# Kernel optimization log

Hardware: AMD Instinct MI355X
Metric: run time of the kernel (lower is better)

The kernel has to match this reference:

```python
import jax, jax.numpy as jnp
import numpy as np

B, T, H, W = 32, 100, 16, 16
CIN, HID, COUT, K = 64, 128, 64, 5
EPS = 1e-3      # keras LayerNormalization default epsilon
ALPHA = 0.2     # LeakyReLU slope


def _conv_same(x, w):
    # x: [B,H,W,Cin], w: [kh,kw,Cin,Cout] -> [B,H,W,Cout], SAME padding, stride 1
    return jax.lax.conv_general_dilated(
        x, w, window_strides=(1, 1), padding='SAME',
        dimension_numbers=('NHWC', 'HWIO', 'NHWC'))


def setup_inputs() -> dict:
    key = jax.random.key(0)
    ks = jax.random.split(key, 8)
    s = 0.05
    return {
        'initial_input': jax.random.normal(ks[0], (B, 1, H, W, CIN), jnp.float32),
        'h0': jax.random.normal(ks[1], (B, H, W, HID), jnp.float32) * s,
        'c0': jax.random.normal(ks[2], (B, H, W, HID), jnp.float32) * s,
        'targets': jax.random.normal(ks[3], (B, T, H, W, CIN), jnp.float32),
        'autoreg_prob': jnp.float32(0.5),
        # ConvLSTM2D params (keras gate order: i, f, c, o stacked on last axis)
        'Wx': jax.random.normal(ks[4], (K, K, CIN, 4 * HID), jnp.float32) * s,
        'Wh': jax.random.normal(ks[5], (K, K, HID, 4 * HID), jnp.float32) * s,
        'b': jnp.zeros((4 * HID,), jnp.float32),
        # Conv2D(64, 3, same)
        'conv_w': jax.random.normal(ks[6], (3, 3, HID, COUT), jnp.float32) * s,
        'conv_b': jnp.zeros((COUT,), jnp.float32),
        # LayerNorm (axis=-1)
        'gamma': jnp.ones((COUT,), jnp.float32),
        'beta': jnp.zeros((COUT,), jnp.float32),
    }


def reference(initial_input, h0, c0, targets, autoreg_prob,
              Wx, Wh, b, conv_w, conv_b, gamma, beta):
    T_ = targets.shape[1]
    t_switch = jnp.float32(T_) * autoreg_prob
    x0 = initial_input[:, 0]                       # [B,H,W,CIN] (seq-len-1 ConvLSTM step)
    tgt_t = jnp.transpose(targets, (1, 0, 2, 3, 4))  # [T,B,H,W,CIN]
    ts = jnp.arange(T_)

    def step(carry, inp):
        x, h, c = carry
        t, tgt = inp
        # ConvLSTM2D cell (one timestep)
        g = _conv_same(x, Wx) + _conv_same(h, Wh) + b   # [B,H,W,4*HID]
        i_g, f_g, c_g, o_g = jnp.split(g, 4, axis=-1)
        c = jax.nn.sigmoid(f_g) * c + jax.nn.sigmoid(i_g) * jnp.tanh(c_g)
        h = jax.nn.sigmoid(o_g) * jnp.tanh(c)
        # Conv2D -> LayerNorm(axis=-1) -> LeakyReLU(0.2)
        y = _conv_same(h, conv_w) + conv_b              # [B,H,W,COUT]
        mu = jnp.mean(y, axis=-1, keepdims=True)
        var = jnp.var(y, axis=-1, keepdims=True)
        y = (y - mu) * jax.lax.rsqrt(var + EPS) * gamma + beta
        out = jnp.where(y >= 0, y, ALPHA * y)
        # autoreg phase feeds output back; teacher phase feeds targets[:, t]
        next_x = jnp.where(t.astype(jnp.float32) < t_switch, out, tgt)
        return (next_x, h, c), out

    _, outs = jax.lax.scan(step, (x0, h0, c0), (ts, tgt_t))
    return jnp.transpose(outs, (1, 0, 2, 3, 4))        # [B,T,H,W,COUT]
```

## Files before the change

### kernel.cpp

```cpp
#include <hip/hip_runtime.h>

#define TT   100
#define PADW 20
#define HID  128
#define CIN  64
#define COUT 64
#define ALPHA 0.2f
#define LNEPS 1e-3f

typedef _Float16 f16;
typedef __attribute__((ext_vector_type(8))) _Float16 f16x8;
typedef __attribute__((ext_vector_type(4))) float f32x4;

__device__ __forceinline__ float fsig(float x) {
  return __builtin_amdgcn_rcpf(1.f + __builtin_amdgcn_exp2f(-1.44269504089f * x));
}
__device__ __forceinline__ float ftanh(float x) {
  return 1.f - 2.f * __builtin_amdgcn_rcpf(1.f + __builtin_amdgcn_exp2f(2.88539008178f * x));
}
__device__ __forceinline__ void gload16(const void* g, void* l) {
  __builtin_amdgcn_global_load_lds((const __attribute__((address_space(1))) void*)g,
                                   (__attribute__((address_space(3))) void*)l,
                                   16, 0, 0);
}

__global__ __launch_bounds__(512, 1) void kA8(
    const f16* __restrict__ Xh, const f16* __restrict__ Xl,
    const f16* __restrict__ Hch, const f16* __restrict__ Hcl,
    f16* __restrict__ Hnh, f16* __restrict__ Hnl,
    const f16* __restrict__ Wch, const f16* __restrict__ Wcl,
    const float* __restrict__ bp, float* __restrict__ cst) {
  __shared__ __align__(16) char smem[126976];
  f16* haloh = (f16*)(smem);
  f16* halol = (f16*)(smem + 30720);
  f16 (*sBh)[128][64] = (f16(*)[128][64])(smem + 61440);
  f16 (*sBl)[128][64] = (f16(*)[128][64])(smem + 94208);
  float* macc = (float*)smem;

  const int tid = threadIdx.x;
  const int l = tid & 63, w = tid >> 6;
  const int h = w & 1, q = w >> 1;
  const int qm = q >> 1, qn = q & 1;
  const int xcd = blockIdx.x & 7, slot = blockIdx.x >> 3;
  const int ni = xcd >> 1;
  const int mi = ((xcd & 1) << 5) + slot;
  const int b_img = mi >> 1;
  const int ybase = (mi & 1) * 8;

  const int cof = ((l & 7) ^ (l >> 3)) * 8;
  int wBo[2];
#pragma unroll
  for (int i = 0; i < 2; ++i) wBo[i] = (ni * 128 + w * 16 + i * 8 + (l >> 3)) * 192 + cof;

  auto stageHalo = [&](int sub) {
#pragma unroll
    for (int i2 = 0; i2 < 4; ++i2) {
      const int gi = w * 4 + i2;
      if (gi < 30) {
        const int sabs = gi * 64 + l;
        const int pix = sabs >> 3, slot3 = sabs & 7;
        const int hrow = pix / 20, hcol = pix - hrow * 20;
        const int sc = slot3 ^ (hcol & 7);
        const int gp = (b_img * PADW + ybase + hrow) * PADW + hcol;
        if (sub == 0) {
          gload16(Xh + gp * CIN + sc * 8, haloh + gi * 512);
          gload16(Xl + gp * CIN + sc * 8, halol + gi * 512);
        } else {
          const int ho = (sub - 1) * 64 + sc * 8;
          gload16(Hch + gp * HID + ho, haloh + gi * 512);
          gload16(Hcl + gp * HID + ho, halol + gi * 512);
        }
      }
    }
  };
  auto stageB = [&](int bf, int tap, int sub) {
    const int wo = tap * (512 * 192) + sub * 64;
#pragma unroll
    for (int i = 0; i < 2; ++i) {
      gload16(Wch + wBo[i] + wo, &sBh[bf][w * 16 + i * 8][0]);
      gload16(Wcl + wBo[i] + wo, &sBl[bf][w * 16 + i * 8][0]);
    }
  };

  f32x4 acc[4][4] = {};

  stageHalo(0);
  stageB(0, 0, 0);
  __syncthreads();

  const int kc8 = h * 4 + (l >> 4);
  const int co = (kc8 ^ (l & 7)) * 8;

  int bufb = 0;
  for (int sub = 0; sub < 3; ++sub) {
    if (sub) {
      stageHalo(sub);
      __syncthreads();
    }
    for (int tap = 0; tap < 25; ++tap) {
      if (tap + 1 < 25) stageB(bufb ^ 1, tap + 1, sub);
      else if (sub + 1 < 3) stageB(bufb ^ 1, 0, sub + 1);
      const int dy = tap / 5, dx = tap - dy * 5;
      const int hcol = (l & 15) + dx;
      const int slot3 = kc8 ^ (hcol & 7);
      const int aoff0 = ((qm * 4 + dy) * 20 + hcol) * 64 + slot3 * 8;
      f16x8 avh[4], avl[4], bvh[4], bvl[4];
#pragma unroll
      for (int fm = 0; fm < 4; ++fm) {
        avh[fm] = *(const f16x8*)&haloh[aoff0 + fm * 1280];
        avl[fm] = *(const f16x8*)&halol[aoff0 + fm * 1280];
      }
#pragma unroll
      for (int fn = 0; fn < 4; ++fn) {
        bvh[fn] = *(const f16x8*)&sBh[bufb][qn * 64 + fn * 16 + (l & 15)][co];
        bvl[fn] = *(const f16x8*)&sBl[bufb][qn * 64 + fn * 16 + (l & 15)][co];
      }
#pragma unroll
      for (int fm = 0; fm < 4; ++fm)
#pragma unroll
        for (int fn = 0; fn < 4; ++fn) {
          acc[fm][fn] =
              __builtin_amdgcn_mfma_f32_16x16x32_f16(avh[fm], bvh[fn], acc[fm][fn], 0, 0, 0);
          acc[fm][fn] =
              __builtin_amdgcn_mfma_f32_16x16x32_f16(avl[fm], bvh[fn], acc[fm][fn], 0, 0, 0);
          acc[fm][fn] =
              __builtin_amdgcn_mfma_f32_16x16x32_f16(avh[fm], bvl[fn], acc[fm][fn], 0, 0, 0);
        }
      __syncthreads();
      bufb ^= 1;
    }
  }

  if (h == 1) {
#pragma unroll
    for (int fm = 0; fm < 4; ++fm)
#pragma unroll
      for (int fn = 0; fn < 4; ++fn)
#pragma unroll
        for (int j = 0; j < 4; ++j)
          macc[q * 4096 + ((fm * 4 + fn) * 4 + j) * 64 + l] = acc[fm][fn][j];
  }
  __syncthreads();
  if (h == 0) {
#pragma unroll
    for (int fm = 0; fm < 4; ++fm)
#pragma unroll
      for (int fn = 0; fn < 4; ++fn)
#pragma unroll
        for (int j = 0; j < 4; ++j)
          acc[fm][fn][j] += macc[q * 4096 + ((fm * 4 + fn) * 4 + j) * 64 + l];

#pragma unroll
    for (int fn = 0; fn < 4; ++fn) {
      const int col = ni * 128 + qn * 64 + fn * 16 + (l & 15);
      const float bias = bp[col];
      const int ch = col >> 2;
#pragma unroll
      for (int fm = 0; fm < 4; ++fm) {
#pragma unroll
        for (int j = 0; j < 4; ++j) {
          const float v = acc[fm][fn][j] + bias;
          const float t1 = __shfl_xor(v, 1);
          const float t2 = __shfl_xor(v, 2);
          const float t3 = __shfl_xor(t1, 2);
          if ((l & 3) == 0) {
            const int m = mi * 128 + qm * 64 + fm * 16 + ((l >> 4) << 2) + j;
            const int cidx = m * HID + ch;
            const float cold = cst[cidx];
            const float cn = fsig(t1) * cold + fsig(v) * ftanh(t2);
            cst[cidx] = cn;
            const float hh_ = fsig(t3) * ftanh(cn);
            const int b = m >> 8, y = (m >> 4) & 15, x = m & 15;
            const int pidx = ((b * PADW + y + 2) * PADW + (x + 2)) * HID + ch;
            const f16 hv = (f16)hh_;
            Hnh[pidx] = hv;
            Hnl[pidx] = (f16)(hh_ - (float)hv);
          }
        }
      }
    }
  }
}

__global__ __launch_bounds__(256, 2) void kB(
    const f16* __restrict__ Hnh, const f16* __restrict__ Hnl,
    const f16* __restrict__ Cwh, const f16* __restrict__ Cwl,
    const float* __restrict__ cb, const float* __restrict__ gam,
    const float* __restrict__ bet, const float* __restrict__ tgt,
    const float* __restrict__ prob, float* __restrict__ outp,
    f16* __restrict__ Xph, f16* __restrict__ Xpl, int t) {
  __shared__ __align__(16) f16 sAh[2][32][64];
  __shared__ __align__(16) f16 sAl[2][32][64];
  __shared__ __align__(16) f16 sBh[2][64][64];
  __shared__ __align__(16) f16 sBl[2][64][64];
  __shared__ __align__(16) float yl[32][68];
  const int tid = threadIdx.x;
  const int l = tid & 63, w = tid >> 6;
  const int wm = w >> 1, wn = w & 1;
  const int mi = blockIdx.x;
  const int cof = ((l & 7) ^ (l >> 3)) * 8;

  const int rA = w * 8 + (l >> 3);
  const int mA = mi * 32 + rA;
  const int bA = mA >> 8, yA = (mA >> 4) & 15, xA = mA & 15;
  const int posA = (bA * PADW + yA + 2) * PADW + (xA + 2);
  int wBo[2];
#pragma unroll
  for (int i = 0; i < 2; ++i) wBo[i] = (w * 16 + i * 8 + (l >> 3)) * HID + cof;

  auto stage = [&](int bf, int it) {
    const int tap = it >> 1, sub = it & 1;
    const int dy = tap / 3, dx = tap - dy * 3;
    const int dt = (dy - 1) * PADW + (dx - 1);
    gload16(Hnh + (posA + dt) * HID + sub * 64 + cof, &sAh[bf][w * 8][0]);
    gload16(Hnl + (posA + dt) * HID + sub * 64 + cof, &sAl[bf][w * 8][0]);
    const int wo = tap * (64 * HID) + sub * 64;
#pragma unroll
    for (int i = 0; i < 2; ++i) {
      gload16(Cwh + wBo[i] + wo, &sBh[bf][w * 16 + i * 8][0]);
      gload16(Cwl + wBo[i] + wo, &sBl[bf][w * 16 + i * 8][0]);
    }
  };

  f32x4 acc[2] = {};

  stage(0, 0);
  __syncthreads();

  int buf = 0;
  for (int it = 0; it < 18; ++it) {
    if (it < 17) stage(buf ^ 1, it + 1);
#pragma unroll
    for (int kk = 0; kk < 2; ++kk) {
      const int co = ((kk * 4 + (l >> 4)) ^ (l & 7)) * 8;
      const f16x8 ah = *(const f16x8*)&sAh[buf][wm * 16 + (l & 15)][co];
      const f16x8 al = *(const f16x8*)&sAl[buf][wm * 16 + (l & 15)][co];
#pragma unroll
      for (int fn = 0; fn < 2; ++fn) {
        const f16x8 bh = *(const f16x8*)&sBh[buf][wn * 32 + fn * 16 + (l & 15)][co];
        const f16x8 bl = *(const f16x8*)&sBl[buf][wn * 32 + fn * 16 + (l & 15)][co];
        acc[fn] = __builtin_amdgcn_mfma_f32_16x16x32_f16(ah, bh, acc[fn], 0, 0, 0);
        acc[fn] = __builtin_amdgcn_mfma_f32_16x16x32_f16(al, bh, acc[fn], 0, 0, 0);
        acc[fn] = __builtin_amdgcn_mfma_f32_16x16x32_f16(ah, bl, acc[fn], 0, 0, 0);
      }
    }
    __syncthreads();
    buf ^= 1;
  }

#pragma unroll
  for (int fn = 0; fn < 2; ++fn) {
    const int col = wn * 32 + fn * 16 + (l & 15);
    const float bias = cb[col];
#pragma unroll
    for (int j = 0; j < 4; ++j) yl[wm * 16 + (l >> 4) * 4 + j][col] = acc[fn][j] + bias;
  }
  __syncthreads();

  if (tid < 128) {
    const int row = tid >> 2, part = tid & 3;
    f32x4 vv[4];
    float s = 0.f, q = 0.f;
#pragma unroll
    for (int k2 = 0; k2 < 4; ++k2) {
      vv[k2] = *(const f32x4*)&yl[row][part * 16 + k2 * 4];
#pragma unroll
      for (int e = 0; e < 4; ++e) { const float f = vv[k2][e]; s += f; q += f * f; }
    }
    s += __shfl_xor(s, 1); q += __shfl_xor(q, 1);
    s += __shfl_xor(s, 2); q += __shfl_xor(q, 2);
    const float mean = s * 0.015625f;
    const float var = q * 0.015625f - mean * mean;
    const float rs = __builtin_amdgcn_rsqf(fmaxf(var, 0.f) + LNEPS);
    const int m = mi * 32 + row;
    const int b = m >> 8, pos = m & 255;
    const int py = pos >> 4, px = pos & 15;
    const long obase = (((long)b * TT + t) * 256 + pos) * COUT + part * 16;
    float* op = outp + obase;
    const float* tp = tgt + obase;
    const bool ar = (float)t < 100.f * prob[0];
    const int xoff = ((b * PADW + py + 2) * PADW + px + 2) * CIN + part * 16;
    f16x8 ph[2], pl[2];
#pragma unroll
    for (int k2 = 0; k2 < 4; ++k2) {
      f32x4 o4;
#pragma unroll
      for (int e = 0; e < 4; ++e) {
        const int c = part * 16 + k2 * 4 + e;
        float val = (vv[k2][e] - mean) * rs * gam[c] + bet[c];
        val = val >= 0.f ? val : ALPHA * val;
        o4[e] = val;
        const float nxt = ar ? val : tp[k2 * 4 + e];
        const f16 nh = (f16)nxt;
        const int i16 = k2 * 4 + e;
        ph[i16 >> 3][i16 & 7] = nh;
        pl[i16 >> 3][i16 & 7] = (f16)(nxt - (float)nh);
      }
      *(f32x4*)(op + k2 * 4) = o4;
    }
    *(f16x8*)(Xph + xoff) = ph[0];
    *(f16x8*)(Xph + xoff + 8) = ph[1];
    *(f16x8*)(Xpl + xoff) = pl[0];
    *(f16x8*)(Xpl + xoff + 8) = pl[1];
  }
}

__global__ void k_wcomb(const float* __restrict__ Wx, const float* __restrict__ Wh,
                        f16* __restrict__ Wch, f16* __restrict__ Wcl) {
  const int idx = blockIdx.x * 256 + threadIdx.x;
  if (idx >= 25 * 512 * 192) return;
  const int c = idx % 192, r = idx / 192;
  const int n = r % 512, tap = r / 512;
  const int ch = n >> 2, g = n & 3, no = g * 128 + ch;
  const float v = (c < 64) ? Wx[(tap * 64 + c) * 512 + no]
                           : Wh[(tap * 128 + (c - 64)) * 512 + no];
  const f16 vh = (f16)v;
  Wch[idx] = vh;
  Wcl[idx] = (f16)(v - (float)vh);
}
__global__ void k_wconv(const float* __restrict__ cw, f16* __restrict__ Cwh,
                        f16* __restrict__ Cwl) {
  const int idx = blockIdx.x * 256 + threadIdx.x;
  if (idx >= 9 * 64 * 128) return;
  const int c = idx % 128, r = idx / 128;
  const int n = r % 64, tap = r / 64;
  const float v = cw[(tap * 128 + c) * 64 + n];
  const f16 vh = (f16)v;
  Cwh[idx] = vh;
  Cwl[idx] = (f16)(v - (float)vh);
}
__global__ void k_bperm(const float* __restrict__ b, float* __restrict__ bp) {
  const int n = blockIdx.x * 256 + threadIdx.x;
  if (n < 512) bp[n] = b[(n & 3) * 128 + (n >> 2)];
}
__global__ void k_init(const float* __restrict__ x0, const float* __restrict__ h0,
                       const float* __restrict__ c0, f16* __restrict__ Xph,
                       f16* __restrict__ Xpl, f16* __restrict__ Hh, f16* __restrict__ Hl,
                       float* __restrict__ cst) {
  const int idx = blockIdx.x * 256 + threadIdx.x;
  if (idx < 32 * 256 * 64) {
    const int ch = idx & 63, m = idx >> 6;
    const int b = m >> 8, y = (m >> 4) & 15, x = m & 15;
    const int p = ((b * PADW + y + 2) * PADW + x + 2) * CIN + ch;
    const float v = x0[idx];
    const f16 vh = (f16)v;
    Xph[p] = vh;
    Xpl[p] = (f16)(v - (float)vh);
  } else if (idx < 32 * 256 * 64 + 32 * 256 * 128) {
    const int j = idx - 32 * 256 * 64;
    const int ch = j & 127, m = j >> 7;
    const int b = m >> 8, y = (m >> 4) & 15, x = m & 15;
    const int p = ((b * PADW + y + 2) * PADW + x + 2) * HID + ch;
    const float v = h0[j];
    const f16 vh = (f16)v;
    Hh[p] = vh;
    Hl[p] = (f16)(v - (float)vh);
  } else if (idx < 32 * 256 * 64 + 2 * 32 * 256 * 128) {
    const int j = idx - 32 * 256 * 64 - 32 * 256 * 128;
    cst[j] = c0[j];
  }
}

extern "C" void kernel_launch(void* const* d_in, const int* in_sizes, int n_in,
                              void* d_out, int out_size, void* d_ws, size_t ws_size,
                              hipStream_t stream) {
  (void)in_sizes; (void)n_in; (void)out_size; (void)ws_size;
  const float* x0  = (const float*)d_in[0];
  const float* h0  = (const float*)d_in[1];
  const float* c0  = (const float*)d_in[2];
  const float* tgt = (const float*)d_in[3];
  const float* pr  = (const float*)d_in[4];
  const float* Wx  = (const float*)d_in[5];
  const float* Wh  = (const float*)d_in[6];
  const float* bb  = (const float*)d_in[7];
  const float* cw  = (const float*)d_in[8];
  const float* cbv = (const float*)d_in[9];
  const float* gam = (const float*)d_in[10];
  const float* bet = (const float*)d_in[11];
  float* outp = (float*)d_out;
  char* ws = (char*)d_ws;
  f16*   Xph = (f16*)(ws + 0);
  f16*   Xpl = (f16*)(ws + 1638400);
  f16*   Hh0 = (f16*)(ws + 3276800);
  f16*   Hl0 = (f16*)(ws + 6553600);
  f16*   Hh1 = (f16*)(ws + 9830400);
  f16*   Hl1 = (f16*)(ws + 13107200);
  float* cst = (float*)(ws + 16384000);
  f16*   Wch = (f16*)(ws + 20578304);
  f16*   Wcl = (f16*)(ws + 25493504);
  f16*   Cwh = (f16*)(ws + 30408704);
  f16*   Cwl = (f16*)(ws + 30556160);
  float* bp  = (float*)(ws + 30703616);

  hipMemsetAsync(Xph, 0, 1638400, stream);
  hipMemsetAsync(Xpl, 0, 1638400, stream);
  hipMemsetAsync(Hh0, 0, 3276800, stream);
  hipMemsetAsync(Hl0, 0, 3276800, stream);
  hipMemsetAsync(Hh1, 0, 3276800, stream);
  hipMemsetAsync(Hl1, 0, 3276800, stream);
  k_wcomb<<<9600, 256, 0, stream>>>(Wx, Wh, Wch, Wcl);
  k_wconv<<<288, 256, 0, stream>>>(cw, Cwh, Cwl);
  k_bperm<<<2, 256, 0, stream>>>(bb, bp);
  k_init<<<10240, 256, 0, stream>>>(x0, h0, c0, Xph, Xpl, Hh0, Hl0, cst);

  for (int t = 0; t < TT; ++t) {
    f16* hch = (t & 1) ? Hh1 : Hh0;
    f16* hcl = (t & 1) ? Hl1 : Hl0;
    f16* hnh = (t & 1) ? Hh0 : Hh1;
    f16* hnl = (t & 1) ? Hl0 : Hl1;
    kA8<<<256, 512, 0, stream>>>(Xph, Xpl, hch, hcl, hnh, hnl, Wch, Wcl, bp, cst);
    kB<<<256, 256, 0, stream>>>(hnh, hnl, Cwh, Cwl, cbv, gam, bet, tgt, pr, outp, Xph, Xpl, t);
  }
}
```

Measured before the change: 12.72 ms.

## Give each warp private weight buffers to drop per-tap block barriers

Reassigns the gate-conv GEMM tiling so each warp pair owns a 32-column N slice across all 128 M rows, instead of a 64x64 quadrant. Each warp now stages its own weight slice into a private double-buffered LDS region. This lets the per-tap __syncthreads be replaced by a per-wave s_waitcnt vmcnt, so block-wide barriers only occur at sub-chunk boundaries. The cost is that each wave reads more A fragments from the halo, and the correctness of the cross-wave LDS reuse now depends on hand-placed waitcnt and barrier calls.

```diff
diff --git a/kernel.cpp b/kernel.cpp
--- a/kernel.cpp
+++ b/kernel.cpp
@@ -24,7 +24,7 @@
                                    16, 0, 0);
 }
 
-__global__ __launch_bounds__(512, 1) void kA8(
+__global__ __launch_bounds__(512, 1) void kA9(
     const f16* __restrict__ Xh, const f16* __restrict__ Xl,
     const f16* __restrict__ Hch, const f16* __restrict__ Hcl,
     f16* __restrict__ Hnh, f16* __restrict__ Hnl,
@@ -33,24 +33,16 @@
   __shared__ __align__(16) char smem[126976];
   f16* haloh = (f16*)(smem);
   f16* halol = (f16*)(smem + 30720);
-  f16 (*sBh)[128][64] = (f16(*)[128][64])(smem + 61440);
-  f16 (*sBl)[128][64] = (f16(*)[128][64])(smem + 94208);
   float* macc = (float*)smem;
 
   const int tid = threadIdx.x;
   const int l = tid & 63, w = tid >> 6;
-  const int h = w & 1, q = w >> 1;
-  const int qm = q >> 1, qn = q & 1;
+  const int h = w & 1, ns = w >> 1;
   const int xcd = blockIdx.x & 7, slot = blockIdx.x >> 3;
   const int ni = xcd >> 1;
   const int mi = ((xcd & 1) << 5) + slot;
   const int b_img = mi >> 1;
   const int ybase = (mi & 1) * 8;
-
-  const int cof = ((l & 7) ^ (l >> 3)) * 8;
-  int wBo[2];
-#pragma unroll
-  for (int i = 0; i < 2; ++i) wBo[i] = (ni * 128 + w * 16 + i * 8 + (l >> 3)) * 192 + cof;
 
   auto stageHalo = [&](int sub) {
 #pragma unroll
@@ -73,90 +65,94 @@
       }
     }
   };
+
+  const int nbase = (ni * 128 + ns * 32) * 192;
+  const int scB = ((l & 3) ^ ((l >> 3) & 3)) * 8;
   auto stageB = [&](int bf, int tap, int sub) {
-    const int wo = tap * (512 * 192) + sub * 64;
+    const int base = tap * (512 * 192) + nbase + sub * 64 + h * 32 + scB;
+    f16* dst = (f16*)(smem + 61440 + w * 8192 + bf * 4096);
 #pragma unroll
     for (int i = 0; i < 2; ++i) {
-      gload16(Wch + wBo[i] + wo, &sBh[bf][w * 16 + i * 8][0]);
-      gload16(Wcl + wBo[i] + wo, &sBl[bf][w * 16 + i * 8][0]);
+      const int so = (i * 16 + (l >> 2)) * 192;
+      gload16(Wch + base + so, dst + i * 512);
+      gload16(Wcl + base + so, dst + 1024 + i * 512);
     }
   };
 
-  f32x4 acc[4][4] = {};
-
-  stageHalo(0);
-  stageB(0, 0, 0);
-  __syncthreads();
+  f32x4 acc[8][2] = {};
 
   const int kc8 = h * 4 + (l >> 4);
-  const int co = (kc8 ^ (l & 7)) * 8;
-
-  int bufb = 0;
+  const int rcB = ((l >> 4) ^ (((l & 15) >> 1) & 3)) * 8;
+  const int rB0 = (l & 15) * 32;
+  const int rB1 = (16 + (l & 15)) * 32;
+
+  int cur = 0;
   for (int sub = 0; sub < 3; ++sub) {
-    if (sub) {
-      stageHalo(sub);
-      __syncthreads();
-    }
+    if (sub) __builtin_amdgcn_s_barrier();
+    stageHalo(sub);
+    stageB(cur, 0, sub);
+    asm volatile("s_waitcnt vmcnt(0)" ::: "memory");
+    __builtin_amdgcn_s_barrier();
     for (int tap = 0; tap < 25; ++tap) {
-      if (tap + 1 < 25) stageB(bufb ^ 1, tap + 1, sub);
-      else if (sub + 1 < 3) stageB(bufb ^ 1, 0, sub + 1);
+      stageB(cur ^ 1, (tap < 24) ? tap + 1 : 24, sub);
+      asm volatile("s_waitcnt vmcnt(4)" ::: "memory");
       const int dy = tap / 5, dx = tap - dy * 5;
       const int hcol = (l & 15) + dx;
       const int slot3 = kc8 ^ (hcol & 7);
-      const int aoff0 = ((qm * 4 + dy) * 20 + hcol) * 64 + slot3 * 8;
-      f16x8 avh[4], avl[4], bvh[4], bvl[4];
-#pragma unroll
-      for (int fm = 0; fm < 4; ++fm) {
-        avh[fm] = *(const f16x8*)&haloh[aoff0 + fm * 1280];
-        avl[fm] = *(const f16x8*)&halol[aoff0 + fm * 1280];
+      const int abase = (dy * 20 + hcol) * 64 + slot3 * 8;
+      const f16* bufB = (const f16*)(smem + 61440 + w * 8192 + cur * 4096);
+      f16x8 bvh[2], bvl[2];
+      bvh[0] = *(const f16x8*)&bufB[rB0 + rcB];
+      bvh[1] = *(const f16x8*)&bufB[rB1 + rcB];
+      bvl[0] = *(const f16x8*)&bufB[1024 + rB0 + rcB];
+      bvl[1] = *(const f16x8*)&bufB[1024 + rB1 + rcB];
+#pragma unroll
+      for (int fm = 0; fm < 8; ++fm) {
+        const f16x8 avh = *(const f16x8*)&haloh[abase + fm * 1280];
+        const f16x8 avl = *(const f16x8*)&halol[abase + fm * 1280];
+#pragma unroll
+        for (int fn = 0; fn < 2; ++fn) {
+          acc[fm][fn] =
+              __builtin_amdgcn_mfma_f32_16x16x32_f16(avh, bvh[fn], acc[fm][fn], 0, 0, 0);
+          acc[fm][fn] =
+              __builtin_amdgcn_mfma_f32_16x16x32_f16(avl, bvh[fn], acc[fm][fn], 0, 0, 0);
+          acc[fm][fn] =
+              __builtin_amdgcn_mfma_f32_16x16x32_f16(avh, bvl[fn], acc[fm][fn], 0, 0, 0);
+        }
       }
-#pragma unroll
-      for (int fn = 0; fn < 4; ++fn) {
-        bvh[fn] = *(const f16x8*)&sBh[bufb][qn * 64 + fn * 16 + (l & 15)][co];
-        bvl[fn] = *(const f16x8*)&sBl[bufb][qn * 64 + fn * 16 + (l & 15)][co];
-      }
-#pragma unroll
-      for (int fm = 0; fm < 4; ++fm)
-#pragma unroll
-        for (int fn = 0; fn < 4; ++fn) {
-          acc[fm][fn] =
-              __builtin_amdgcn_mfma_f32_16x16x32_f16(avh[fm], bvh[fn], acc[fm][fn], 0, 0, 0);
-          acc[fm][fn] =
-              __builtin_amdgcn_mfma_f32_16x16x32_f16(avl[fm], bvh[fn], acc[fm][fn], 0, 0, 0);
-          acc[fm][fn] =
-              __builtin_amdgcn_mfma_f32_16x16x32_f16(avh[fm], bvl[fn], acc[fm][fn], 0, 0, 0);
-        }
-      __syncthreads();
-      bufb ^= 1;
-    }
-  }
+      cur ^= 1;
+    }
+  }
+
+  asm volatile("s_waitcnt vmcnt(0)" ::: "memory");
+  __builtin_amdgcn_s_barrier();
 
   if (h == 1) {
 #pragma unroll
-    for (int fm = 0; fm < 4; ++fm)
-#pragma unroll
-      for (int fn = 0; fn < 4; ++fn)
+    for (int fm = 0; fm < 8; ++fm)
+#pragma unroll
+      for (int fn = 0; fn < 2; ++fn)
 #pragma unroll
         for (int j = 0; j < 4; ++j)
-          macc[q * 4096 + ((fm * 4 + fn) * 4 + j) * 64 + l] = acc[fm][fn][j];
+          macc[ns * 4096 + ((fm * 2 + fn) * 4 + j) * 64 + l] = acc[fm][fn][j];
   }
   __syncthreads();
   if (h == 0) {
 #pragma unroll
-    for (int fm = 0; fm < 4; ++fm)
-#pragma unroll
-      for (int fn = 0; fn < 4; ++fn)
+    for (int fm = 0; fm < 8; ++fm)
+#pragma unroll
+      for (int fn = 0; fn < 2; ++fn)
 #pragma unroll
         for (int j = 0; j < 4; ++j)
-          acc[fm][fn][j] += macc[q * 4096 + ((fm * 4 + fn) * 4 + j) * 64 + l];
-
-#pragma unroll
-    for (int fn = 0; fn < 4; ++fn) {
-      const int col = ni * 128 + qn * 64 + fn * 16 + (l & 15);
+          acc[fm][fn][j] += macc[ns * 4096 + ((fm * 2 + fn) * 4 + j) * 64 + l];
+
+#pragma unroll
+    for (int fn = 0; fn < 2; ++fn) {
+      const int col = ni * 128 + ns * 32 + fn * 16 + (l & 15);
       const float bias = bp[col];
       const int ch = col >> 2;
 #pragma unroll
-      for (int fm = 0; fm < 4; ++fm) {
+      for (int fm = 0; fm < 8; ++fm) {
 #pragma unroll
         for (int j = 0; j < 4; ++j) {
           const float v = acc[fm][fn][j] + bias;
@@ -164,7 +160,7 @@
           const float t2 = __shfl_xor(v, 2);
           const float t3 = __shfl_xor(t1, 2);
           if ((l & 3) == 0) {
-            const int m = mi * 128 + qm * 64 + fm * 16 + ((l >> 4) << 2) + j;
+            const int m = mi * 128 + fm * 16 + ((l >> 4) << 2) + j;
             const int cidx = m * HID + ch;
             const float cold = cst[cidx];
             const float cn = fsig(t1) * cold + fsig(v) * ftanh(t2);
@@ -408,7 +404,7 @@
     f16* hcl = (t & 1) ? Hl1 : Hl0;
     f16* hnh = (t & 1) ? Hh0 : Hh1;
     f16* hnl = (t & 1) ? Hl0 : Hl1;
-    kA8<<<256, 512, 0, stream>>>(Xph, Xpl, hch, hcl, hnh, hnl, Wch, Wcl, bp, cst);
+    kA9<<<256, 512, 0, stream>>>(Xph, Xpl, hch, hcl, hnh, hnl, Wch, Wcl, bp, cst);
     kB<<<256, 256, 0, stream>>>(hnh, hnl, Cwh, Cwl, cbv, gam, bet, tgt, pr, outp, Xph, Xpl, t);
   }
 }
```

Result: slower. 13.01 ms (+2.3%).
